# Performance work log

Hardware: AMD Instinct MI355X
Metric: run time of the kernel (lower is better)

Reference implementation:

```python
import jax, jax.numpy as jnp
import numpy as np

B, C, O, N, T, K = 4, 64, 64, 32768, 4, 9
PAD, DIL = 4, 1  # padding*dilation, dilation
SIGMA = 0.05
EPS_BN = 1e-5


def _gather_ch(x, idx):
    # x: [B, C, N], idx: [B, N] -> gather along last dim per channel
    idx3 = jnp.broadcast_to(idx[:, None, :], x.shape)
    return jnp.take_along_axis(x, idx3, axis=-1)


def _weighted_conv(x, coords, w):
    # x: [B,C,N], coords: [B,3,N], w: [O,C,K]
    xp = jnp.pad(x, ((0, 0), (0, 0), (PAD, PAD)))
    cp = jnp.pad(coords, ((0, 0), (0, 0), (PAD, PAD)))
    win_idx = jnp.arange(N)[:, None] + jnp.arange(K) * DIL  # [N, K]
    win = xp[:, :, win_idx]   # [B,C,N,K]
    cwin = cp[:, :, win_idx]  # [B,3,N,K]
    d = cwin - cwin[:, :, :, K // 2:K // 2 + 1]
    s = jnp.sum(d * d, axis=1)                    # [B,N,K]
    r = jnp.sqrt(jnp.where(s > 0, s, 1.0))
    r = jnp.where(s > 0, r, 0.0)
    wgt = jnp.maximum(1.0 - r / SIGMA, 0.0)       # [B,N,K]
    return jnp.einsum('bcnk,bnk,ock->bon', win, wgt, w)


def _bn(x, g, b):
    # training-mode BatchNorm1d over (B, N)
    m = jnp.mean(x, axis=(0, 2), keepdims=True)
    v = jnp.var(x, axis=(0, 2), keepdims=True)
    return g[None, :, None] * (x - m) * jax.lax.rsqrt(v + EPS_BN) + b[None, :, None]


def setup_inputs() -> dict:
    key = jax.random.key(0)
    ks = jax.random.split(key, 12)
    inp = jax.random.normal(ks[0], (B, C, N), dtype=jnp.float32)
    # coords in a small box so sigma=0.05 yields non-trivial weights
    multi_coords = jax.random.uniform(ks[1], (B, 3, N, T), dtype=jnp.float32) * 0.02
    indices = jax.random.randint(ks[2], (B, N, T), 0, N, dtype=jnp.int32)
    reindices = jax.random.randint(ks[3], (B, N, T), 0, N, dtype=jnp.int32)
    fan = C * K
    conv_w = jax.random.normal(ks[4], (T, O, C, K), dtype=jnp.float32) / np.sqrt(fan)
    bn_gamma = jnp.ones((T, O), dtype=jnp.float32)
    bn_beta = jnp.zeros((T, O), dtype=jnp.float32)
    fusion_w = jax.random.normal(ks[5], (O, T * O), dtype=jnp.float32) / np.sqrt(T * O)
    fusion_b = jnp.zeros((O,), dtype=jnp.float32)
    fusion_gamma = jnp.ones((O,), dtype=jnp.float32)
    fusion_beta = jnp.zeros((O,), dtype=jnp.float32)
    return {"input": inp, "multi_coords": multi_coords, "indices": indices,
            "reindices": reindices, "conv_w": conv_w, "bn_gamma": bn_gamma,
            "bn_beta": bn_beta, "fusion_w": fusion_w, "fusion_b": fusion_b,
            "fusion_gamma": fusion_gamma, "fusion_beta": fusion_beta}


def reference(input, multi_coords, indices, reindices, conv_w, bn_gamma, bn_beta,
              fusion_w, fusion_b, fusion_gamma, fusion_beta):
    outs = []
    for i in range(T):  # fixed small set of 4 Hilbert orders
        x = _gather_ch(input, indices[:, :, i])            # [B,C,N]
        x = _weighted_conv(x, multi_coords[:, :, :, i], conv_w[i])  # [B,O,N]
        x = _bn(x, bn_gamma[i], bn_beta[i])
        x = _gather_ch(x, reindices[:, :, i])
        outs.append(x)
    cat = jnp.concatenate(outs, axis=1)                    # [B, T*O, N]
    y = jnp.einsum('bcn,oc->bon', cat, fusion_w) + fusion_b[None, :, None]
    y = _bn(y, fusion_gamma, fusion_beta)
    return jax.nn.relu(y)
```

## Files before the change

kernel.cpp:

```cpp
#include <hip/hip_runtime.h>
#include <hip/hip_bf16.h>

#define BB 4
#define CC 64
#define OO 64
#define NN 32768
#define TT 4
#define KK 9
#define PADW 4
#define SIGMA 0.05f
#define EPS_BN 1e-5f

typedef __attribute__((ext_vector_type(8))) short bf16x8;
typedef __attribute__((ext_vector_type(4))) float f32x4;

__device__ __forceinline__ unsigned short f2bf(float f) {
  __hip_bfloat16 h = __float2bfloat16(f);
  return *reinterpret_cast<unsigned short*>(&h);
}
__device__ __forceinline__ float bf2f(unsigned short u) {
  unsigned int x = ((unsigned int)u) << 16;
  float f;
  __builtin_memcpy(&f, &x, 4);
  return f;
}
__device__ __forceinline__ unsigned int pkbf(float a, float b) {
  float2 t; t.x = a; t.y = b;
  __hip_bfloat162 h = __float22bfloat162_rn(t);
  unsigned int r;
  __builtin_memcpy(&r, &h, 4);
  return r;
}

__global__ __launch_bounds__(256) void transpose_kernel(
    const float* __restrict__ inp, unsigned short* __restrict__ xTb)
{
  const int n0 = blockIdx.x * 64;
  const int b  = blockIdx.y;
  const int tid = threadIdx.x;
  __shared__ float xt[64][65];
  {
    int nl = tid & 63, c4 = tid >> 6;
    #pragma unroll
    for (int i = 0; i < 16; ++i) {
      int c = c4 * 16 + i;
      xt[c][nl] = inp[((size_t)(b*CC + c))*NN + n0 + nl];
    }
  }
  __syncthreads();
  {
    int nl = tid >> 2, cq = tid & 3;
    unsigned int pk[8];
    #pragma unroll
    for (int i = 0; i < 8; ++i) {
      int c = cq*16 + i*2;
      pk[i] = pkbf(xt[c][nl], xt[c+1][nl]);
    }
    unsigned int* dst = (unsigned int*)(xTb + (((size_t)b*NN) + n0 + nl)*CC + cq*16);
    ((int4*)dst)[0] = make_int4((int)pk[0],(int)pk[1],(int)pk[2],(int)pk[3]);
    ((int4*)dst)[1] = make_int4((int)pk[4],(int)pk[5],(int)pk[6],(int)pk[7]);
  }
}

__global__ __launch_bounds__(256) void wprep_kernel(
    const float* __restrict__ cw, unsigned short* __restrict__ W4)
{
  const int k = blockIdx.x;
  const int t = blockIdx.y;
  for (int u = threadIdx.x; u < OO*CC; u += 256) {
    int o = u >> 6, c = u & 63;
    int ow = o >> 5, ot = (o >> 4) & 1, l15 = o & 15;
    int frag = c >> 5, q = (c >> 3) & 3, j = c & 7;
    float wv = cw[(((size_t)(t*OO + o))*CC + c)*KK + k];
    W4[(size_t)(t*9+k)*4096 + ow*2048 + ot*1024 + frag*512 + l15*32 + q*8 + j]
        = f2bf(wv);
  }
}

__global__ __launch_bounds__(256, 4) void conv_kernel(
    const unsigned short* __restrict__ xTb,
    const float* __restrict__ mc,
    const int*   __restrict__ ind,
    const unsigned short* __restrict__ W4,
    unsigned short* __restrict__ Y,
    float* __restrict__ cpart2)
{
  const int n0  = blockIdx.x * 128;
  const int b   = blockIdx.y;
  const int t   = blockIdx.z;
  const int tid = threadIdx.x;
  const int lane = tid & 63;
  const int w    = tid >> 6;
  const int l15  = lane & 15;
  const int q    = lane >> 4;
  const int ow   = w & 1;
  const int nw   = w >> 1;

  __shared__ short xg[136*64];
  __shared__ float wgl[128][10];
  __shared__ float mcs[3][140];

  int idxr[5];
  #pragma unroll
  for (int i = 0; i < 5; ++i) {
    int u = tid + 256*i;
    int p = u >> 3;
    int m = n0 + p - PADW;
    idxr[i] = -1;
    if (u < 1088 && m >= 0 && m < NN)
      idxr[i] = ind[((size_t)b*NN + m)*TT + t];
  }

  int4 g[5];
  #pragma unroll
  for (int i = 0; i < 5; ++i) {
    int s = (tid + 256*i) & 7;
    g[i] = make_int4(0,0,0,0);
    if (idxr[i] >= 0)
      g[i] = *(const int4*)(xTb + ((size_t)b*NN + idxr[i])*CC + s*8);
  }

  if (tid < 136) {
    int m = n0 + tid - PADW;
    #pragma unroll
    for (int d = 0; d < 3; ++d) {
      float4 v = make_float4(0.f, 0.f, 0.f, 0.f);
      if (m >= 0 && m < NN)
        v = *(const float4*)(mc + (((size_t)(b*3+d))*NN + m)*TT);
      mcs[d][tid] = (t==0) ? v.x : (t==1) ? v.y : (t==2) ? v.z : v.w;
    }
  }

  #pragma unroll
  for (int i = 0; i < 5; ++i) {
    int u = tid + 256*i;
    if (u < 1088) {
      int p = u >> 3, s = u & 7;
      *(int4*)&xg[(p << 6) + ((s ^ (p & 7)) << 3)] = g[i];
    }
  }
  __syncthreads();

  {
    int nl = tid >> 1;
    int k0 = (tid & 1) * 5;
    int kc = 5 - (tid & 1);
    float cx = mcs[0][nl+4], cy = mcs[1][nl+4], cz = mcs[2][nl+4];
    for (int i2 = 0; i2 < kc; ++i2) {
      int k = k0 + i2, mi = nl + k;
      float dx = mcs[0][mi]-cx, dy = mcs[1][mi]-cy, dz = mcs[2][mi]-cz;
      float s2 = dx*dx + dy*dy + dz*dz;
      float r = (s2 > 0.f) ? sqrtf(s2) : 0.f;
      wgl[nl][k] = fmaxf(1.f - r*(1.f/SIGMA), 0.f);
    }
  }
  __syncthreads();

  const unsigned short* Wt = W4 + (size_t)t*9*4096 + ow*2048 + (l15*4 + q)*8;
  const f32x4 Z = {0.f, 0.f, 0.f, 0.f};
  f32x4 fin[2][4];
  #pragma unroll
  for (int ot = 0; ot < 2; ++ot)
    #pragma unroll
    for (int ns = 0; ns < 4; ++ns) fin[ot][ns] = Z;

  for (int k = 0; k < KK; ++k) {
    const unsigned short* Wk = Wt + (size_t)k*4096;
    bf16x8 af[2][2];
    #pragma unroll
    for (int ot = 0; ot < 2; ++ot) {
      af[ot][0] = *(const bf16x8*)(Wk + ot*1024);
      af[ot][1] = *(const bf16x8*)(Wk + ot*1024 + 512);
    }
    #pragma unroll
    for (int ns = 0; ns < 4; ++ns) {
      int nl = nw*64 + ns*16 + l15;
      int p  = nl + k;
      const short* row = &xg[p << 6];
      int sw = p & 7;
      bf16x8 b0 = *(const bf16x8*)(row + ((q ^ sw) << 3));
      bf16x8 b1 = *(const bf16x8*)(row + (((4 + q) ^ sw) << 3));
      float wgt = wgl[nl][k];
      #pragma unroll
      for (int ot = 0; ot < 2; ++ot) {
        f32x4 d = __builtin_amdgcn_mfma_f32_16x16x32_bf16(af[ot][0], b0, Z, 0, 0, 0);
        d = __builtin_amdgcn_mfma_f32_16x16x32_bf16(af[ot][1], b1, d, 0, 0, 0);
        fin[ot][ns] += wgt * d;
      }
    }
  }

  #pragma unroll
  for (int ns = 0; ns < 4; ++ns) {
    int nl = nw*64 + ns*16 + l15;
    size_t row = (((size_t)t*BB + b)*NN + n0 + nl)*OO;
    #pragma unroll
    for (int ot = 0; ot < 2; ++ot) {
      uint2 pk2;
      pk2.x = pkbf(fin[ot][ns][0], fin[ot][ns][1]);
      pk2.y = pkbf(fin[ot][ns][2], fin[ot][ns][3]);
      *(uint2*)(Y + row + ow*32 + ot*16 + q*4) = pk2;
    }
  }

  float sv[16];
  #pragma unroll
  for (int ot = 0; ot < 2; ++ot)
    #pragma unroll
    for (int r = 0; r < 4; ++r) {
      float a = 0.f, qs = 0.f;
      #pragma unroll
      for (int ns = 0; ns < 4; ++ns) {
        float v = fin[ot][ns][r];
        a += v; qs += v*v;
      }
      sv[ot*4+r] = a; sv[8+ot*4+r] = qs;
    }
  #pragma unroll
  for (int msk = 1; msk < 16; msk <<= 1) {
    #pragma unroll
    for (int i = 0; i < 16; ++i) sv[i] += __shfl_xor(sv[i], msk, 16);
  }
  if (l15 == 0) {
    int slot4 = ((b*256 + (int)blockIdx.x) << 2) | w;
    #pragma unroll
    for (int ot = 0; ot < 2; ++ot)
      #pragma unroll
      for (int r = 0; r < 4; ++r) {
        int o = ow*32 + ot*16 + q*4 + r;
        cpart2[((size_t)((t*64 + o)*2 + 0))*4096 + slot4] = sv[ot*4+r];
        cpart2[((size_t)((t*64 + o)*2 + 1))*4096 + slot4] = sv[8+ot*4+r];
      }
  }
}

__global__ __launch_bounds__(256) void bnparam_kernel(
    const float* __restrict__ cpart2,
    const float* __restrict__ gam,
    const float* __restrict__ bet,
    float* __restrict__ ss)
{
  const int to = blockIdx.x;
  const int tid = threadIdx.x;
  __shared__ float r1[256], r2[256];
  const float* p1 = cpart2 + (size_t)to*2*4096;
  const float* p2 = p1 + 4096;
  float s1 = 0.f, s2 = 0.f;
  for (int i = tid*4; i < 4096; i += 1024) {
    float4 a = *(const float4*)(p1 + i);
    float4 c = *(const float4*)(p2 + i);
    s1 += a.x + a.y + a.z + a.w;
    s2 += c.x + c.y + c.z + c.w;
  }
  r1[tid] = s1; r2[tid] = s2;
  __syncthreads();
  for (int st = 128; st > 0; st >>= 1) {
    if (tid < st) { r1[tid] += r1[tid+st]; r2[tid] += r2[tid+st]; }
    __syncthreads();
  }
  if (tid == 0) {
    const float inv = 1.f / (float)(BB * NN);
    float mean = r1[0] * inv;
    float var  = r2[0] * inv - mean * mean;
    float sc = gam[to] * rsqrtf(var + EPS_BN);
    ss[to*2 + 0] = sc;
    ss[to*2 + 1] = bet[to] - mean * sc;
  }
}

__global__ __launch_bounds__(256) void wfuse_kernel(
    const float* __restrict__ fw,
    const float* __restrict__ fb,
    const float* __restrict__ ss,
    float* __restrict__ fbp)
{
  const int tid = threadIdx.x;
  int o = tid >> 2, c0 = (tid & 3) * 64;
  float s = 0.f;
  for (int c = c0; c < c0 + 64; ++c)
    s += fw[o*256 + c] * ss[c*2 + 1];
  s += __shfl_xor(s, 1);
  s += __shfl_xor(s, 2);
  if ((tid & 3) == 0) fbp[o] = fb[o] + s;
}

__global__ __launch_bounds__(256, 4) void fusion_kernel(
    const unsigned short* __restrict__ Y,
    const int*   __restrict__ rind,
    const float* __restrict__ ss,
    const float* __restrict__ fw,
    const float* __restrict__ fbp,
    float* __restrict__ out,
    float* __restrict__ fpart2)
{
  const int n0  = blockIdx.x * 128;
  const int b   = blockIdx.y;
  const int tid = threadIdx.x;
  const int lane = tid & 63;
  const int w    = tid >> 6;
  const int l15  = lane & 15;
  const int q    = lane >> 4;
  const int ow   = w & 1;
  const int nw   = w >> 1;

  __shared__ short zg[128*64];
  __shared__ float scl[256];

  scl[tid] = ss[tid*2];

  int4 rg[4];
  #pragma unroll
  for (int i = 0; i < 4; ++i) {
    int n = (tid >> 3) + 32*i;
    rg[i] = *(const int4*)(rind + ((size_t)b*NN + n0 + n)*TT);
  }

  f32x4 fin[2][4];
  #pragma unroll
  for (int ot = 0; ot < 2; ++ot)
    #pragma unroll
    for (int ns = 0; ns < 4; ++ns) fin[ot][ns] = (f32x4){0.f,0.f,0.f,0.f};

  #pragma unroll
  for (int r = 0; r < 4; ++r) {
    if (r) __syncthreads();
    #pragma unroll
    for (int i = 0; i < 4; ++i) {
      int u = tid + 256*i;
      int n = u >> 3, s = u & 7;
      int rn = (r == 0) ? rg[i].x : (r == 1) ? rg[i].y
             : (r == 2) ? rg[i].z : rg[i].w;
      int4 raw = *(const int4*)(Y + (((size_t)r*BB + b)*NN + rn)*OO + s*8);
      *(int4*)&zg[(n << 6) + ((s ^ (n & 7)) << 3)] = raw;
    }
    __syncthreads();

    #pragma unroll
    for (int kk = 0; kk < 2; ++kk) {
      bf16x8 af[2];
      #pragma unroll
      for (int ot = 0; ot < 2; ++ot) {
        int o = ow*32 + ot*16 + l15;
        int cb = r*64 + kk*32 + q*8;
        const float* wp = fw + (size_t)o*256 + cb;
        float4 wa = *(const float4*)wp;
        float4 wb = *(const float4*)(wp + 4);
        unsigned int u0 = pkbf(wa.x*scl[cb+0], wa.y*scl[cb+1]);
        unsigned int u1 = pkbf(wa.z*scl[cb+2], wa.w*scl[cb+3]);
        unsigned int u2 = pkbf(wb.x*scl[cb+4], wb.y*scl[cb+5]);
        unsigned int u3 = pkbf(wb.z*scl[cb+6], wb.w*scl[cb+7]);
        int4 tmp = make_int4((int)u0,(int)u1,(int)u2,(int)u3);
        __builtin_memcpy(&af[ot], &tmp, 16);
      }
      #pragma unroll
      for (int ns = 0; ns < 4; ++ns) {
        int nl = nw*64 + ns*16 + l15;
        int ch = (kk*4 + q) ^ (nl & 7);
        bf16x8 bfr = *(const bf16x8*)&zg[(nl << 6) + (ch << 3)];
        #pragma unroll
        for (int ot = 0; ot < 2; ++ot)
          fin[ot][ns] = __builtin_amdgcn_mfma_f32_16x16x32_bf16(af[ot], bfr, fin[ot][ns], 0, 0, 0);
      }
    }
  }

  float sv[16];
  #pragma unroll
  for (int ot = 0; ot < 2; ++ot)
    #pragma unroll
    for (int r2 = 0; r2 < 4; ++r2) {
      int o = ow*32 + ot*16 + q*4 + r2;
      float bias = fbp[o];
      float* dst = out + ((size_t)(b*OO + o))*NN + n0 + nw*64;
      float a = 0.f, qs = 0.f;
      #pragma unroll
      for (int ns = 0; ns < 4; ++ns) {
        float v = fin[ot][ns][r2] + bias;
        dst[ns*16 + l15] = v;
        a += v; qs += v*v;
      }
      sv[ot*4+r2] = a; sv[8+ot*4+r2] = qs;
    }
  #pragma unroll
  for (int msk = 1; msk < 16; msk <<= 1) {
    #pragma unroll
    for (int i = 0; i < 16; ++i) sv[i] += __shfl_xor(sv[i], msk, 16);
  }
  if (l15 == 0) {
    int slot4 = ((b*256 + (int)blockIdx.x) << 2) | w;
    #pragma unroll
    for (int ot = 0; ot < 2; ++ot)
      #pragma unroll
      for (int r2 = 0; r2 < 4; ++r2) {
        int o = ow*32 + ot*16 + q*4 + r2;
        fpart2[((size_t)(o*2 + 0))*4096 + slot4] = sv[ot*4+r2];
        fpart2[((size_t)(o*2 + 1))*4096 + slot4] = sv[8+ot*4+r2];
      }
  }
}

__global__ __launch_bounds__(256) void freduce_kernel(
    const float* __restrict__ fpart2,
    const float* __restrict__ fg,
    const float* __restrict__ fbeta,
    float* __restrict__ fss)
{
  const int o = blockIdx.x;
  const int tid = threadIdx.x;
  __shared__ float r1[256], r2[256];
  const float* p1 = fpart2 + (size_t)o*2*4096;
  const float* p2 = p1 + 4096;
  float s1 = 0.f, s2 = 0.f;
  for (int i = tid*4; i < 4096; i += 1024) {
    float4 a = *(const float4*)(p1 + i);
    float4 c = *(const float4*)(p2 + i);
    s1 += a.x + a.y + a.z + a.w;
    s2 += c.x + c.y + c.z + c.w;
  }
  r1[tid] = s1; r2[tid] = s2;
  __syncthreads();
  for (int st = 128; st > 0; st >>= 1) {
    if (tid < st) { r1[tid] += r1[tid+st]; r2[tid] += r2[tid+st]; }
    __syncthreads();
  }
  if (tid == 0) {
    const float inv = 1.f / (float)(BB * NN);
    float mean = r1[0] * inv;
    float var  = r2[0] * inv - mean * mean;
    float sc = fg[o] * rsqrtf(var + EPS_BN);
    fss[o*2 + 0] = sc;
    fss[o*2 + 1] = fbeta[o] - mean * sc;
  }
}

__global__ __launch_bounds__(256) void final_kernel(
    float* __restrict__ out, const float* __restrict__ fss)
{
  const int e0 = blockIdx.x * 2048 + threadIdx.x;
  #pragma unroll
  for (int s = 0; s < 8; ++s) {
    int e  = e0 + s * 256;
    int o2 = (e >> 15) & 63;
    float sc = fss[o2*2 + 0];
    float sh = fss[o2*2 + 1];
    float v = out[e] * sc + sh;
    out[e] = fmaxf(v, 0.f);
  }
}

extern "C" void kernel_launch(void* const* d_in, const int* in_sizes, int n_in,
                              void* d_out, int out_size, void* d_ws, size_t ws_size,
                              hipStream_t stream) {
  const float* inp  = (const float*)d_in[0];
  const float* mc   = (const float*)d_in[1];
  const int*   ind  = (const int*)  d_in[2];
  const int*   rind = (const int*)  d_in[3];
  const float* cw   = (const float*)d_in[4];
  const float* bg   = (const float*)d_in[5];
  const float* bb   = (const float*)d_in[6];
  const float* fw   = (const float*)d_in[7];
  const float* fb   = (const float*)d_in[8];
  const float* fg   = (const float*)d_in[9];
  const float* fbt  = (const float*)d_in[10];

  char* ws = (char*)d_ws;
  float* convss = (float*)(ws + 0);
  float* fss    = (float*)(ws + 2048);
  float* fbp    = (float*)(ws + 3072);
  unsigned short* Y = (unsigned short*)(ws + 8192);
  float* fpart2 = (float*)(ws + 8192 + 67108864);

  char* ob = (char*)d_out;
  unsigned short* xTb = (unsigned short*)ob;
  unsigned short* W4  = (unsigned short*)(ob + 16777216);
  float*          cpart2 = (float*)(ob + 17072128);
  float* out = (float*)d_out;

  dim3 gt(NN/64, BB);
  transpose_kernel<<<gt, 256, 0, stream>>>(inp, xTb);

  dim3 gw(KK, TT);
  wprep_kernel<<<gw, 256, 0, stream>>>(cw, W4);

  dim3 gc(NN/128, BB, TT);
  conv_kernel<<<gc, 256, 0, stream>>>(xTb, mc, ind, W4, Y, cpart2);

  bnparam_kernel<<<256, 256, 0, stream>>>(cpart2, bg, bb, convss);

  wfuse_kernel<<<1, 256, 0, stream>>>(fw, fb, convss, fbp);

  dim3 gf(NN/128, BB);
  fusion_kernel<<<gf, 256, 0, stream>>>(Y, rind, convss, fw, fbp, out, fpart2);

  freduce_kernel<<<OO, 256, 0, stream>>>(fpart2, fg, fbt, fss);

  final_kernel<<<(BB*OO*NN)/2048, 256, 0, stream>>>(out, fss);
}
```

Baseline: 232.0 us.

## Double conv tile to 256 points and precompute scaled bf16 fusion weights

The conv kernel now processes 256 points per block instead of 128. This halves the halo overhead and reuses each weight fragment load across twice as many MFMA tiles, at the cost of more registers and LDS (launch bounds lowered to 3 blocks per CU). The BN-partial slot layout and the bnparam reduction length are adjusted to match. Separately, wfuse_kernel now precomputes BN-scaled fusion weights in bf16, already in MFMA fragment layout, so fusion_kernel loads them directly instead of rescaling and converting them in every block.

```diff
diff --git a/kernel.cpp b/kernel.cpp
--- a/kernel.cpp
+++ b/kernel.cpp
@@ -18,12 +18,6 @@
   __hip_bfloat16 h = __float2bfloat16(f);
   return *reinterpret_cast<unsigned short*>(&h);
 }
-__device__ __forceinline__ float bf2f(unsigned short u) {
-  unsigned int x = ((unsigned int)u) << 16;
-  float f;
-  __builtin_memcpy(&f, &x, 4);
-  return f;
-}
 __device__ __forceinline__ unsigned int pkbf(float a, float b) {
   float2 t; t.x = a; t.y = b;
   __hip_bfloat162 h = __float22bfloat162_rn(t);
@@ -77,7 +71,7 @@
   }
 }
 
-__global__ __launch_bounds__(256, 4) void conv_kernel(
+__global__ __launch_bounds__(256, 3) void conv_kernel(
     const unsigned short* __restrict__ xTb,
     const float* __restrict__ mc,
     const int*   __restrict__ ind,
@@ -85,7 +79,7 @@
     unsigned short* __restrict__ Y,
     float* __restrict__ cpart2)
 {
-  const int n0  = blockIdx.x * 128;
+  const int n0  = blockIdx.x * 256;
   const int b   = blockIdx.y;
   const int t   = blockIdx.z;
   const int tid = threadIdx.x;
@@ -96,45 +90,45 @@
   const int ow   = w & 1;
   const int nw   = w >> 1;
 
-  __shared__ short xg[136*64];
-  __shared__ float wgl[128][10];
-  __shared__ float mcs[3][140];
-
-  int idxr[5];
-  #pragma unroll
-  for (int i = 0; i < 5; ++i) {
+  __shared__ short xg[264*64];
+  __shared__ float wgl[256][10];
+  __shared__ float mcs[3][268];
+
+  int idxr[9];
+  #pragma unroll
+  for (int i = 0; i < 9; ++i) {
     int u = tid + 256*i;
     int p = u >> 3;
     int m = n0 + p - PADW;
     idxr[i] = -1;
-    if (u < 1088 && m >= 0 && m < NN)
+    if (u < 2112 && m >= 0 && m < NN)
       idxr[i] = ind[((size_t)b*NN + m)*TT + t];
   }
 
-  int4 g[5];
-  #pragma unroll
-  for (int i = 0; i < 5; ++i) {
+  int4 g[9];
+  #pragma unroll
+  for (int i = 0; i < 9; ++i) {
     int s = (tid + 256*i) & 7;
     g[i] = make_int4(0,0,0,0);
     if (idxr[i] >= 0)
       g[i] = *(const int4*)(xTb + ((size_t)b*NN + idxr[i])*CC + s*8);
   }
 
-  if (tid < 136) {
-    int m = n0 + tid - PADW;
+  for (int u = tid; u < 264; u += 256) {
+    int m = n0 + u - PADW;
     #pragma unroll
     for (int d = 0; d < 3; ++d) {
       float4 v = make_float4(0.f, 0.f, 0.f, 0.f);
       if (m >= 0 && m < NN)
         v = *(const float4*)(mc + (((size_t)(b*3+d))*NN + m)*TT);
-      mcs[d][tid] = (t==0) ? v.x : (t==1) ? v.y : (t==2) ? v.z : v.w;
-    }
-  }
-
-  #pragma unroll
-  for (int i = 0; i < 5; ++i) {
+      mcs[d][u] = (t==0) ? v.x : (t==1) ? v.y : (t==2) ? v.z : v.w;
+    }
+  }
+
+  #pragma unroll
+  for (int i = 0; i < 9; ++i) {
     int u = tid + 256*i;
-    if (u < 1088) {
+    if (u < 2112) {
       int p = u >> 3, s = u & 7;
       *(int4*)&xg[(p << 6) + ((s ^ (p & 7)) << 3)] = g[i];
     }
@@ -142,13 +136,11 @@
   __syncthreads();
 
   {
-    int nl = tid >> 1;
-    int k0 = (tid & 1) * 5;
-    int kc = 5 - (tid & 1);
+    int nl = tid;
     float cx = mcs[0][nl+4], cy = mcs[1][nl+4], cz = mcs[2][nl+4];
-    for (int i2 = 0; i2 < kc; ++i2) {
-      int k = k0 + i2, mi = nl + k;
-      float dx = mcs[0][mi]-cx, dy = mcs[1][mi]-cy, dz = mcs[2][mi]-cz;
+    #pragma unroll
+    for (int k = 0; k < KK; ++k) {
+      float dx = mcs[0][nl+k]-cx, dy = mcs[1][nl+k]-cy, dz = mcs[2][nl+k]-cz;
       float s2 = dx*dx + dy*dy + dz*dz;
       float r = (s2 > 0.f) ? sqrtf(s2) : 0.f;
       wgl[nl][k] = fmaxf(1.f - r*(1.f/SIGMA), 0.f);
@@ -158,11 +150,11 @@
 
   const unsigned short* Wt = W4 + (size_t)t*9*4096 + ow*2048 + (l15*4 + q)*8;
   const f32x4 Z = {0.f, 0.f, 0.f, 0.f};
-  f32x4 fin[2][4];
+  f32x4 fin[2][8];
   #pragma unroll
   for (int ot = 0; ot < 2; ++ot)
     #pragma unroll
-    for (int ns = 0; ns < 4; ++ns) fin[ot][ns] = Z;
+    for (int ns = 0; ns < 8; ++ns) fin[ot][ns] = Z;
 
   for (int k = 0; k < KK; ++k) {
     const unsigned short* Wk = Wt + (size_t)k*4096;
@@ -173,8 +165,8 @@
       af[ot][1] = *(const bf16x8*)(Wk + ot*1024 + 512);
     }
     #pragma unroll
-    for (int ns = 0; ns < 4; ++ns) {
-      int nl = nw*64 + ns*16 + l15;
+    for (int ns = 0; ns < 8; ++ns) {
+      int nl = nw*128 + ns*16 + l15;
       int p  = nl + k;
       const short* row = &xg[p << 6];
       int sw = p & 7;
@@ -191,8 +183,8 @@
   }
 
   #pragma unroll
-  for (int ns = 0; ns < 4; ++ns) {
-    int nl = nw*64 + ns*16 + l15;
+  for (int ns = 0; ns < 8; ++ns) {
+    int nl = nw*128 + ns*16 + l15;
     size_t row = (((size_t)t*BB + b)*NN + n0 + nl)*OO;
     #pragma unroll
     for (int ot = 0; ot < 2; ++ot) {
@@ -210,7 +202,7 @@
     for (int r = 0; r < 4; ++r) {
       float a = 0.f, qs = 0.f;
       #pragma unroll
-      for (int ns = 0; ns < 4; ++ns) {
+      for (int ns = 0; ns < 8; ++ns) {
         float v = fin[ot][ns][r];
         a += v; qs += v*v;
       }
@@ -222,7 +214,7 @@
     for (int i = 0; i < 16; ++i) sv[i] += __shfl_xor(sv[i], msk, 16);
   }
   if (l15 == 0) {
-    int slot4 = ((b*256 + (int)blockIdx.x) << 2) | w;
+    int slot4 = ((b*128 + (int)blockIdx.x) << 2) | w;
     #pragma unroll
     for (int ot = 0; ot < 2; ++ot)
       #pragma unroll
@@ -246,7 +238,7 @@
   const float* p1 = cpart2 + (size_t)to*2*4096;
   const float* p2 = p1 + 4096;
   float s1 = 0.f, s2 = 0.f;
-  for (int i = tid*4; i < 4096; i += 1024) {
+  for (int i = tid*4; i < 2048; i += 1024) {
     float4 a = *(const float4*)(p1 + i);
     float4 c = *(const float4*)(p2 + i);
     s1 += a.x + a.y + a.z + a.w;
@@ -272,23 +264,35 @@
     const float* __restrict__ fw,
     const float* __restrict__ fb,
     const float* __restrict__ ss,
-    float* __restrict__ fbp)
-{
-  const int tid = threadIdx.x;
-  int o = tid >> 2, c0 = (tid & 3) * 64;
-  float s = 0.f;
-  for (int c = c0; c < c0 + 64; ++c)
-    s += fw[o*256 + c] * ss[c*2 + 1];
-  s += __shfl_xor(s, 1);
-  s += __shfl_xor(s, 2);
-  if ((tid & 3) == 0) fbp[o] = fb[o] + s;
+    float* __restrict__ fbp,
+    unsigned short* __restrict__ FWB)
+{
+  const int tid = threadIdx.x;
+  {
+    int o = tid >> 2, c0 = (tid & 3) * 64;
+    float s = 0.f;
+    for (int c = c0; c < c0 + 64; ++c)
+      s += fw[o*256 + c] * ss[c*2 + 1];
+    s += __shfl_xor(s, 1);
+    s += __shfl_xor(s, 2);
+    if ((tid & 3) == 0) fbp[o] = fb[o] + s;
+  }
+  for (int e = tid; e < 16384; e += 256) {
+    int rk  = e >> 11;
+    int ow  = (e >> 10) & 1;
+    int ot  = (e >> 9) & 1;
+    int l15 = (e >> 5) & 15;
+    int cj  = e & 31;
+    int o = ow*32 + ot*16 + l15;
+    int c = (rk >> 1)*64 + (rk & 1)*32 + cj;
+    FWB[e] = f2bf(fw[o*256 + c] * ss[c*2]);
+  }
 }
 
 __global__ __launch_bounds__(256, 4) void fusion_kernel(
     const unsigned short* __restrict__ Y,
     const int*   __restrict__ rind,
-    const float* __restrict__ ss,
-    const float* __restrict__ fw,
+    const unsigned short* __restrict__ FWB,
     const float* __restrict__ fbp,
     float* __restrict__ out,
     float* __restrict__ fpart2)
@@ -304,9 +308,6 @@
   const int nw   = w >> 1;
 
   __shared__ short zg[128*64];
-  __shared__ float scl[256];
-
-  scl[tid] = ss[tid*2];
 
   int4 rg[4];
   #pragma unroll
@@ -337,21 +338,11 @@
 
     #pragma unroll
     for (int kk = 0; kk < 2; ++kk) {
+      int rk = r*2 + kk;
+      const unsigned short* wp = FWB + rk*2048 + ow*1024 + (l15*4 + q)*8;
       bf16x8 af[2];
-      #pragma unroll
-      for (int ot = 0; ot < 2; ++ot) {
-        int o = ow*32 + ot*16 + l15;
-        int cb = r*64 + kk*32 + q*8;
-        const float* wp = fw + (size_t)o*256 + cb;
-        float4 wa = *(const float4*)wp;
-        float4 wb = *(const float4*)(wp + 4);
-        unsigned int u0 = pkbf(wa.x*scl[cb+0], wa.y*scl[cb+1]);
-        unsigned int u1 = pkbf(wa.z*scl[cb+2], wa.w*scl[cb+3]);
-        unsigned int u2 = pkbf(wb.x*scl[cb+4], wb.y*scl[cb+5]);
-        unsigned int u3 = pkbf(wb.z*scl[cb+6], wb.w*scl[cb+7]);
-        int4 tmp = make_int4((int)u0,(int)u1,(int)u2,(int)u3);
-        __builtin_memcpy(&af[ot], &tmp, 16);
-      }
+      af[0] = *(const bf16x8*)(wp);
+      af[1] = *(const bf16x8*)(wp + 512);
       #pragma unroll
       for (int ns = 0; ns < 4; ++ns) {
         int nl = nw*64 + ns*16 + l15;
@@ -469,6 +460,7 @@
   float* fbp    = (float*)(ws + 3072);
   unsigned short* Y = (unsigned short*)(ws + 8192);
   float* fpart2 = (float*)(ws + 8192 + 67108864);
+  unsigned short* FWB = (unsigned short*)(ws + 8192 + 67108864 + 2097152);
 
   char* ob = (char*)d_out;
   unsigned short* xTb = (unsigned short*)ob;
@@ -482,15 +474,15 @@
   dim3 gw(KK, TT);
   wprep_kernel<<<gw, 256, 0, stream>>>(cw, W4);
 
-  dim3 gc(NN/128, BB, TT);
+  dim3 gc(NN/256, BB, TT);
   conv_kernel<<<gc, 256, 0, stream>>>(xTb, mc, ind, W4, Y, cpart2);
 
   bnparam_kernel<<<256, 256, 0, stream>>>(cpart2, bg, bb, convss);
 
-  wfuse_kernel<<<1, 256, 0, stream>>>(fw, fb, convss, fbp);
+  wfuse_kernel<<<1, 256, 0, stream>>>(fw, fb, convss, fbp, FWB);
 
   dim3 gf(NN/128, BB);
-  fusion_kernel<<<gf, 256, 0, stream>>>(Y, rind, convss, fw, fbp, out, fpart2);
+  fusion_kernel<<<gf, 256, 0, stream>>>(Y, rind, FWB, fbp, out, fpart2);
 
   freduce_kernel<<<OO, 256, 0, stream>>>(fpart2, fg, fbt, fss);
 
```

Result: faster. 223.7 us (-3.6%).
